# Kernel optimization log

Measured on AMD Instinct MI355X. Metric: run time of the kernel, lower is better.

Reference implementation:

```python
import jax, jax.numpy as jnp
import numpy as np

N, D, H = 4096, 1024, 16
HD = D // H  # 64
EPS = 1e-5


def setup_inputs() -> dict:
    key = jax.random.key(0)
    ks = jax.random.split(key, 12)
    lim = 1.0 / np.sqrt(D)
    def lin(kw, kb):
        W = jax.random.uniform(kw, (D, D), jnp.float32, -lim, lim)
        b = jax.random.uniform(kb, (D,), jnp.float32, -lim, lim)
        return W, b
    Wq, bq = lin(ks[0], ks[1])
    Wk, bk = lin(ks[2], ks[3])
    Wv, bv = lin(ks[4], ks[5])
    Wo, bo = lin(ks[6], ks[7])
    return {
        "query": jax.random.normal(ks[8], (N, D), jnp.float32),
        "key": jax.random.normal(ks[9], (N, D), jnp.float32),
        "value": jax.random.normal(ks[10], (N, D), jnp.float32),
        "Wq": Wq, "bq": bq, "Wk": Wk, "bk": bk,
        "Wv": Wv, "bv": bv, "Wo": Wo, "bo": bo,
        "q_norm_w": jnp.ones((HD,), jnp.float32),
        "k_norm_w": jnp.ones((HD,), jnp.float32),
    }


def _rmsnorm(x, w):
    # eqx.nn.RMSNorm: weight-only, eps=1e-5, over last dim
    inv = jax.lax.rsqrt(jnp.mean(x * x, axis=-1, keepdims=True) + EPS)
    return w * x * inv


def reference(query, key, value, Wq, bq, Wk, bk, Wv, bv, Wo, bo, q_norm_w, k_norm_w):
    n = query.shape[0]
    q = (query @ Wq.T + bq).reshape(n, H, HD)
    k = (key @ Wk.T + bk).reshape(n, H, HD)
    v = (value @ Wv.T + bv).reshape(n, H, HD)
    q = _rmsnorm(q, q_norm_w)
    k = _rmsnorm(k, k_norm_w)
    # scale=1.0: raw unscaled dot-product logits
    logits = jnp.einsum('qhd,khd->hqk', q, k)  # [H, N, N]
    probs = jax.nn.softmax(logits, axis=-1)
    attn = jnp.einsum('hqk,khd->qhd', probs, v).reshape(n, H * HD)
    return attn @ Wo.T + bo
```

## Files before the change

### kernel.cpp

```cpp
#include <hip/hip_runtime.h>
#include <stdint.h>
#include <stddef.h>

#define N_TOK 4096
#define DM    1024
#define NHEAD 16
#define HD    64

typedef __attribute__((ext_vector_type(8)))  short bf16x8;
typedef __attribute__((ext_vector_type(4)))  short bf16x4;
typedef __attribute__((ext_vector_type(4)))  float f32x4;
typedef __attribute__((ext_vector_type(16))) float f32x16;

static __device__ __forceinline__ float bf2f(short u) {
  union { unsigned int i; float f; } c;
  c.i = ((unsigned int)(unsigned short)u) << 16;
  return c.f;
}
static __device__ __forceinline__ unsigned short f2bf(float f) {
  union { float f; unsigned int i; } c; c.f = f;
  unsigned int x = c.i;
  return (unsigned short)((x + 0x7fffu + ((x >> 16) & 1u)) >> 16);
}
static __device__ __forceinline__ unsigned int cvtpk(float lo, float hi) {
  unsigned int d;
  asm("v_cvt_pk_bf16_f32 %0, %1, %2" : "=v"(d) : "v"(lo), "v"(hi));
  return d;
}
static __device__ __forceinline__ void plswap(unsigned int& a, unsigned int& b) {
  asm("v_permlane32_swap_b32 %0, %1" : "+v"(a), "+v"(b));
}
#if __has_builtin(__builtin_amdgcn_exp2f)
#define EXP2(x) __builtin_amdgcn_exp2f(x)
#else
#define EXP2(x) exp2f(x)
#endif
static __device__ __forceinline__ void gload16(const void* g, void* l) {
  __builtin_amdgcn_global_load_lds(
      (const __attribute__((address_space(1))) unsigned int*)g,
      (__attribute__((address_space(3))) unsigned int*)l, 16, 0, 0);
}

struct Cvt7 { const float* s[7]; unsigned short* d[7]; };
__global__ void cvt_all(Cvt7 a) {
  int u0 = blockIdx.x << 10;
  int seg, off;
  if (u0 < 1572864) { seg = u0 >> 19; off = u0 & 524287; }
  else { int j = u0 - 1572864; seg = 3 + (j >> 17); off = j & 131071; }
  const float* s = a.s[seg];
  unsigned short* dd = a.d[seg];
  int t = off + threadIdx.x;
#pragma unroll
  for (int j = 0; j < 4; ++j, t += 256) {
    const f32x4* sp = (const f32x4*)(s + (size_t)t * 8);
    f32x4 x = sp[0], y = sp[1];
    bf16x8 o;
    o[0] = (short)f2bf(x[0]); o[1] = (short)f2bf(x[1]);
    o[2] = (short)f2bf(x[2]); o[3] = (short)f2bf(x[3]);
    o[4] = (short)f2bf(y[0]); o[5] = (short)f2bf(y[1]);
    o[6] = (short)f2bf(y[2]); o[7] = (short)f2bf(y[3]);
    *(bf16x8*)(dd + (size_t)t * 8) = o;
  }
}

template <int MI>
static __device__ __forceinline__ void gemm_core(
    const unsigned short* __restrict__ A,
    const unsigned short* __restrict__ W,
    const float* __restrict__ bias,
    unsigned short* __restrict__ Cb,
    float* __restrict__ Cf,
    const float* __restrict__ nw,
    int Nn, int K, int mode, int m0, int n0)
{
  __shared__ __align__(16) unsigned short At[2][MI * 1024];
  __shared__ __align__(16) unsigned short Wt[2][128 * 32];
  const int tid  = threadIdx.x;
  const int wid  = tid >> 6, lane = tid & 63;
  const int lm   = lane & 15, lg = lane >> 4;
  const int wm   = (wid >> 1) * (MI * 16), wn = (wid & 1) * 64;
  const int CPW  = (MI * 2 + 8) / 4;

  f32x4 acc[MI][4];
#pragma unroll
  for (int i = 0; i < MI; ++i)
#pragma unroll
    for (int j = 0; j < 4; ++j) acc[i][j] = f32x4{0.f, 0.f, 0.f, 0.f};

  auto stage = [&](int b, int k0) {
#pragma unroll
    for (int i = 0; i < CPW; ++i) {
      int c = wid * CPW + i;
      if (c < MI * 2)
        gload16(A + (size_t)(m0 + c * 16 + (lane >> 2)) * K + k0 + (lane & 3) * 8,
                (char*)At + b * (MI * 2048) + c * 1024);
      else
        gload16(W + (size_t)(n0 + (c - MI * 2) * 16 + (lane >> 2)) * K + k0 + (lane & 3) * 8,
                (char*)Wt + b * 8192 + (c - MI * 2) * 1024);
    }
  };

  const int nk = K >> 5;
  stage(0, 0);
  __syncthreads();
  for (int kt = 0; kt < nk; ++kt) {
    const int cur = kt & 1;
    if (kt + 1 < nk) stage(cur ^ 1, (kt + 1) << 5);

    bf16x8 af[MI], bfr[4];
#pragma unroll
    for (int mi = 0; mi < MI; ++mi)
      af[mi] = *(const bf16x8*)&At[cur][(wm + mi * 16 + lm) * 32 + lg * 8];
#pragma unroll
    for (int ni = 0; ni < 4; ++ni)
      bfr[ni] = *(const bf16x8*)&Wt[cur][(wn + ni * 16 + lm) * 32 + lg * 8];
    __builtin_amdgcn_s_setprio(1);
#pragma unroll
    for (int mi = 0; mi < MI; ++mi)
#pragma unroll
      for (int ni = 0; ni < 4; ++ni)
        acc[mi][ni] = __builtin_amdgcn_mfma_f32_16x16x32_bf16(
            af[mi], bfr[ni], acc[mi][ni], 0, 0, 0);
    __builtin_amdgcn_s_setprio(0);
    __syncthreads();
  }

  float bv[4];
#pragma unroll
  for (int ni = 0; ni < 4; ++ni) bv[ni] = bias[n0 + wn + ni * 16 + lm];

  if (mode <= 1) {
#pragma unroll
    for (int mi = 0; mi < MI; ++mi)
#pragma unroll
      for (int ni = 0; ni < 4; ++ni) {
        int n = n0 + wn + ni * 16 + lm;
#pragma unroll
        for (int r = 0; r < 4; ++r) {
          int m = m0 + wm + mi * 16 + lg * 4 + r;
          float v = acc[mi][ni][r] + bv[ni];
          if (mode == 1) Cf[(size_t)m * Nn + n] = v;
          else           Cb[(size_t)m * Nn + n] = f2bf(v);
        }
      }
  } else if (mode == 2) {
    const int h = (n0 + wn) >> 6;
    float w_[4];
#pragma unroll
    for (int ni = 0; ni < 4; ++ni) w_[ni] = nw[ni * 16 + lm];
#pragma unroll
    for (int mi = 0; mi < MI; ++mi) {
      float t[4][4], ssq[4];
#pragma unroll
      for (int ni = 0; ni < 4; ++ni)
#pragma unroll
        for (int r = 0; r < 4; ++r) t[ni][r] = acc[mi][ni][r] + bv[ni];
#pragma unroll
      for (int r = 0; r < 4; ++r)
        ssq[r] = t[0][r]*t[0][r] + t[1][r]*t[1][r] + t[2][r]*t[2][r] + t[3][r]*t[3][r];
#pragma unroll
      for (int r = 0; r < 4; ++r) {
        ssq[r] += __shfl_xor(ssq[r], 1);
        ssq[r] += __shfl_xor(ssq[r], 2);
        ssq[r] += __shfl_xor(ssq[r], 4);
        ssq[r] += __shfl_xor(ssq[r], 8);
      }
#pragma unroll
      for (int r = 0; r < 4; ++r) {
        float iv = rsqrtf(ssq[r] * (1.f / 64.f) + 1e-5f);
        int n_ = m0 + wm + mi * 16 + lg * 4 + r;
#pragma unroll
        for (int ni = 0; ni < 4; ++ni) {
          int d = ni * 16 + lm;
          Cb[(size_t)h * (N_TOK * HD) + (size_t)n_ * HD + d] = f2bf(t[ni][r] * w_[ni] * iv);
        }
      }
    }
  } else {
    const int h = (n0 + wn) >> 6;
#pragma unroll
    for (int mi = 0; mi < MI; ++mi)
#pragma unroll
      for (int ni = 0; ni < 4; ++ni) {
        int d  = ni * 16 + lm;
        int nb = m0 + wm + mi * 16 + lg * 4;
        bf16x4 o;
#pragma unroll
        for (int r = 0; r < 4; ++r) o[r] = (short)f2bf(acc[mi][ni][r] + bv[ni]);
        *(bf16x4*)&Cb[(size_t)h * (HD * N_TOK) + (size_t)d * N_TOK + nb] = o;
      }
  }
}

__global__ __launch_bounds__(256, 3) void qkv_gemm(
    const unsigned short* __restrict__ a0, const unsigned short* __restrict__ a1,
    const unsigned short* __restrict__ a2,
    const unsigned short* __restrict__ w0, const unsigned short* __restrict__ w1,
    const unsigned short* __restrict__ w2,
    const float* __restrict__ b0, const float* __restrict__ b1,
    const float* __restrict__ b2,
    unsigned short* __restrict__ o0, unsigned short* __restrict__ o1,
    unsigned short* __restrict__ o2,
    const float* __restrict__ knw)
{
  const int z = blockIdx.z;
  const unsigned short* A = (z == 0) ? a0 : (z == 1) ? a1 : a2;
  const unsigned short* W = (z == 0) ? w0 : (z == 1) ? w1 : w2;
  const float* B          = (z == 0) ? b0 : (z == 1) ? b1 : b2;
  unsigned short* O       = (z == 0) ? o0 : (z == 1) ? o1 : o2;
  const int mode          = (z == 0) ? 0 : (z == 1) ? 2 : 3;
  gemm_core<4>(A, W, B, O, nullptr, knw, DM, DM, mode,
               blockIdx.y * 128, blockIdx.x * 128);
}

__global__ __launch_bounds__(256, 4) void out_gemm(
    const unsigned short* __restrict__ A, const unsigned short* __restrict__ W,
    const float* __restrict__ bias, float* __restrict__ Cf)
{
  gemm_core<2>(A, W, bias, nullptr, Cf, nullptr, DM, DM, 1,
               blockIdx.y * 64, blockIdx.x * 128);
}

__global__ __launch_bounds__(512, 4) void attn_kernel(
    const unsigned short* __restrict__ qb,
    const unsigned short* __restrict__ kn,
    const unsigned short* __restrict__ vt,
    const float* __restrict__ wq,
    unsigned short* __restrict__ ob)
{
  __shared__ __align__(16) unsigned short SM[2][2][2][4096];

  const int wg   = blockIdx.x;
  const int x_   = wg & 7, rest = wg >> 3;
  const int h    = x_ * 2 + (rest & 1);
  const int qt   = rest >> 1;
  const int tid  = threadIdx.x;
  const int wid  = tid >> 6, lane = tid & 63;
  const int g    = wid >> 2, wv = wid & 3;
  const int l31  = lane & 31, hi = lane >> 5;
  const int sl   = l31 & 7;
  const int qbase = qt * 128 + wv * 32;

  bf16x8 qf[4];
  {
    const unsigned short* qp = qb + (size_t)(qbase + l31) * DM + h * HD + hi * 8;
    float qv[32]; float ss = 0.f;
#pragma unroll
    for (int s = 0; s < 4; ++s) {
      bf16x8 raw = *(const bf16x8*)(qp + s * 16);
#pragma unroll
      for (int j = 0; j < 8; ++j) { float f = bf2f(raw[j]); qv[s*8+j] = f; ss += f*f; }
    }
    ss += __shfl_xor(ss, 32);
    float inv = rsqrtf(ss * (1.f / 64.f) + 1e-5f) * 1.44269504f;
#pragma unroll
    for (int s = 0; s < 4; ++s)
#pragma unroll
      for (int j = 0; j < 8; ++j)
        qf[s][j] = (short)f2bf(qv[s*8+j] * wq[s*16 + hi*8 + j] * inv);
  }

  int slot[4];
#pragma unroll
  for (int x = 0; x < 4; ++x) slot[x] = (((2*x + hi) ^ sl) << 4);
  const char* base = (const char*)SM + g * 32768 + l31 * 128;

  const char* gsrc[4];
  char*       ldst[4];
  long        gstep[4];
  {
    const char* knb = (const char*)kn + (size_t)h * (N_TOK * HD * 2);
    const char* vtb = (const char*)vt + (size_t)h * (HD * N_TOK * 2);
    char* smG = (char*)SM + g * 32768;
#pragma unroll
    for (int i = 0; i < 4; ++i) {
      int chunk = wv * 4 + i;
      int off   = (chunk & 7) * 1024 + lane * 16;
      int row   = off >> 7;
      int scol  = (off & 127) ^ ((row & 7) << 4);
      if (chunk < 8) {
        gsrc[i]  = knb + (size_t)(g * 2048 + row) * 128 + scol;
        gstep[i] = 64 * 128;
        ldst[i]  = smG + (chunk & 7) * 1024;
      } else {
        gsrc[i]  = vtb + (size_t)row * (N_TOK * 2) + g * 4096 + scol;
        gstep[i] = 64 * 2;
        ldst[i]  = smG + 8192 + (chunk & 7) * 1024;
      }
    }
  }

  f32x16 oacc[2], fz;
#pragma unroll
  for (int r = 0; r < 16; ++r) { oacc[0][r] = 0.f; oacc[1][r] = 0.f; fz[r] = 0.f; }
  float lsp[4] = {0.f, 0.f, 0.f, 0.f};

#pragma unroll
  for (int i = 0; i < 4; ++i) { gload16(gsrc[i], ldst[i]); gsrc[i] += gstep[i]; }
  __syncthreads();

  const int NT = 2048 / 64;
  for (int it = 0; it < NT; ++it) {
    const int cur = it & 1;
    if (it + 1 < NT) {
      const int nb = cur ^ 1;
#pragma unroll
      for (int i = 0; i < 4; ++i) {
        gload16(gsrc[i], ldst[i] + nb * 16384);
        gsrc[i] += gstep[i];
      }
    }
    const char* KB = base + cur * 16384;
    const char* VB = KB + 8192;

    f32x16 sc[2];
    __builtin_amdgcn_s_setprio(1);
#pragma unroll
    for (int kt = 0; kt < 2; ++kt) {
      bf16x8 kf0 = *(const bf16x8*)(KB + kt * 4096 + slot[0]);
      sc[kt] = __builtin_amdgcn_mfma_f32_32x32x16_bf16(kf0, qf[0], fz, 0, 0, 0);
#pragma unroll
      for (int s = 1; s < 4; ++s) {
        bf16x8 kf = *(const bf16x8*)(KB + kt * 4096 + slot[s]);
        sc[kt] = __builtin_amdgcn_mfma_f32_32x32x16_bf16(kf, qf[s], sc[kt], 0, 0, 0);
      }
    }
    __builtin_amdgcn_s_setprio(0);

#pragma unroll
    for (int kt = 0; kt < 2; ++kt) {
      float e[16];
#pragma unroll
      for (int r = 0; r < 16; ++r) { e[r] = EXP2(sc[kt][r]); lsp[r & 3] += e[r]; }
      unsigned int wpk[4][2];
#pragma unroll
      for (int b = 0; b < 4; ++b) {
        wpk[b][0] = cvtpk(e[4*b+0], e[4*b+1]);
        wpk[b][1] = cvtpk(e[4*b+2], e[4*b+3]);
      }
#pragma unroll
      for (int pr = 0; pr < 2; ++pr) {
        unsigned int x0 = wpk[2*pr][0], x1 = wpk[2*pr][1];
        unsigned int y0 = wpk[2*pr+1][0], y1 = wpk[2*pr+1][1];
        plswap(x0, y0);
        plswap(x1, y1);
        union { unsigned int u[4]; bf16x8 v; } pa;
        pa.u[0] = x0; pa.u[1] = x1; pa.u[2] = y0; pa.u[3] = y1;
        int ks = kt * 2 + pr;
        __builtin_amdgcn_s_setprio(1);
#pragma unroll
        for (int dt = 0; dt < 2; ++dt) {
          bf16x8 vf = *(const bf16x8*)(VB + dt * 4096 + slot[ks]);
          oacc[dt] = __builtin_amdgcn_mfma_f32_32x32x16_bf16(pa.v, vf, oacc[dt], 0, 0, 0);
        }
        __builtin_amdgcn_s_setprio(0);
      }
    }
    __syncthreads();
  }

  float ls = (lsp[0] + lsp[1]) + (lsp[2] + lsp[3]);
  ls += __shfl_xor(ls, 32);

  float* ex  = (float*)((char*)SM + 32768);
  float* lsx = (float*)SM;
  const int idx = wv * 64 + lane;
  if (g == 1) {
#pragma unroll
    for (int dt = 0; dt < 2; ++dt)
#pragma unroll
      for (int r = 0; r < 16; ++r)
        ex[(dt * 16 + r) * 256 + idx] = oacc[dt][r];
    lsx[idx] = ls;
  }
  __syncthreads();
  if (g == 0) {
#pragma unroll
    for (int dt = 0; dt < 2; ++dt)
#pragma unroll
      for (int r = 0; r < 16; ++r)
        oacc[dt][r] += ex[(dt * 16 + r) * 256 + idx];
    ls += lsx[idx];
    float il = 1.f / ls;
#pragma unroll
    for (int r = 0; r < 16; ++r) {
      int q = (r & 3) + 8 * (r >> 2) + 4 * hi;
      float ilr = __int_as_float(
          __builtin_amdgcn_ds_bpermute(q << 2, __float_as_int(il)));
      unsigned short* op = ob + (size_t)(qbase + q) * DM + h * HD + l31;
      op[0]  = f2bf(oacc[0][r] * ilr);
      op[32] = f2bf(oacc[1][r] * ilr);
    }
  }
}

extern "C" void kernel_launch(void* const* d_in, const int* in_sizes, int n_in,
                              void* d_out, int out_size, void* d_ws, size_t ws_size,
                              hipStream_t stream) {
  const float* query = (const float*)d_in[0];
  const float* key   = (const float*)d_in[1];
  const float* value = (const float*)d_in[2];
  const float* Wq    = (const float*)d_in[3];
  const float* bq    = (const float*)d_in[4];
  const float* Wk    = (const float*)d_in[5];
  const float* bk    = (const float*)d_in[6];
  const float* Wv    = (const float*)d_in[7];
  const float* bv    = (const float*)d_in[8];
  const float* Wo    = (const float*)d_in[9];
  const float* bo    = (const float*)d_in[10];
  const float* qnw   = (const float*)d_in[11];
  const float* knw   = (const float*)d_in[12];

  char* ws = (char*)d_ws;
  const size_t MB = 1024 * 1024;
  unsigned short* qpj = (unsigned short*)(ws + 0 * MB);
  unsigned short* Kn  = (unsigned short*)(ws + 8 * MB);
  unsigned short* Vt  = (unsigned short*)(ws + 16 * MB);
  unsigned short* wob = (unsigned short*)(ws + 24 * MB);
  unsigned short* wqb = (unsigned short*)(ws + 26 * MB);
  unsigned short* wkb = (unsigned short*)(ws + 28 * MB);
  unsigned short* wvb = (unsigned short*)(ws + 30 * MB);
  unsigned short* qbf = (unsigned short*)(ws + 32 * MB);
  unsigned short* kbf = (unsigned short*)(ws + 40 * MB);
  unsigned short* vbf = (unsigned short*)(ws + 48 * MB);
  unsigned short* apj = (unsigned short*)(ws + 56 * MB);

  Cvt7 ca;
  ca.s[0] = query; ca.d[0] = qbf;
  ca.s[1] = key;   ca.d[1] = kbf;
  ca.s[2] = value; ca.d[2] = vbf;
  ca.s[3] = Wq;    ca.d[3] = wqb;
  ca.s[4] = Wk;    ca.d[4] = wkb;
  ca.s[5] = Wv;    ca.d[5] = wvb;
  ca.s[6] = Wo;    ca.d[6] = wob;
  cvt_all<<<2048, 256, 0, stream>>>(ca);

  qkv_gemm<<<dim3(DM / 128, N_TOK / 128, 3), 256, 0, stream>>>(
      qbf, kbf, vbf, wqb, wkb, wvb, bq, bk, bv, qpj, Kn, Vt, knw);

  attn_kernel<<<512, 512, 0, stream>>>(qpj, Kn, Vt, qnw, apj);

  out_gemm<<<dim3(DM / 128, N_TOK / 64), 256, 0, stream>>>(apj, wob, bo, (float*)d_out);
}
```

Before: 154.7 us.

## Load V fragments directly from global and stage only K through LDS

V tiles are no longer staged through shared memory. Each lane now reads its V fragments straight from global memory into registers. Only K goes through LDS, using a 4-slot ring that is refilled two tiles at a time, so there is one barrier per two KV tiles instead of one per tile. The aim is to cut LDS traffic and barrier count. In exchange, the direct V loads are strided and uncoalesced and their latency is exposed inside compute, since they are issued at the start of each tile with no prefetch.

```diff
diff --git a/kernel.cpp b/kernel.cpp
--- a/kernel.cpp
+++ b/kernel.cpp
@@ -228,7 +228,7 @@
     const float* __restrict__ wq,
     unsigned short* __restrict__ ob)
 {
-  __shared__ __align__(16) unsigned short SM[2][2][2][4096];
+  __shared__ __align__(16) unsigned short Ksm[2][4][4096];
 
   const int wg   = blockIdx.x;
   const int x_   = wg & 7, rest = wg >> 3;
@@ -263,56 +263,45 @@
   int slot[4];
 #pragma unroll
   for (int x = 0; x < 4; ++x) slot[x] = (((2*x + hi) ^ sl) << 4);
-  const char* base = (const char*)SM + g * 32768 + l31 * 128;
-
-  const char* gsrc[4];
-  char*       ldst[4];
-  long        gstep[4];
+  const char* kbase = (const char*)Ksm + g * 32768 + l31 * 128;
+
+  const char* kgsrc[2];
+  char*       kldst[2];
   {
-    const char* knb = (const char*)kn + (size_t)h * (N_TOK * HD * 2);
-    const char* vtb = (const char*)vt + (size_t)h * (HD * N_TOK * 2);
-    char* smG = (char*)SM + g * 32768;
-#pragma unroll
-    for (int i = 0; i < 4; ++i) {
-      int chunk = wv * 4 + i;
-      int off   = (chunk & 7) * 1024 + lane * 16;
-      int row   = off >> 7;
-      int scol  = (off & 127) ^ ((row & 7) << 4);
-      if (chunk < 8) {
-        gsrc[i]  = knb + (size_t)(g * 2048 + row) * 128 + scol;
-        gstep[i] = 64 * 128;
-        ldst[i]  = smG + (chunk & 7) * 1024;
-      } else {
-        gsrc[i]  = vtb + (size_t)row * (N_TOK * 2) + g * 4096 + scol;
-        gstep[i] = 64 * 2;
-        ldst[i]  = smG + 8192 + (chunk & 7) * 1024;
-      }
-    }
-  }
+    const char* knb = (const char*)kn + (size_t)h * (N_TOK * HD * 2)
+                    + (size_t)g * 2048 * 128;
+#pragma unroll
+    for (int i = 0; i < 2; ++i) {
+      int c    = wv * 2 + i;
+      int off  = c * 1024 + lane * 16;
+      int row  = off >> 7;
+      int scol = (off & 127) ^ ((row & 7) << 4);
+      kgsrc[i] = knb + (size_t)row * 128 + scol;
+      kldst[i] = (char*)Ksm + g * 32768 + c * 1024;
+    }
+  }
+  const unsigned short* vb0 = vt + ((size_t)h * HD + l31) * N_TOK + g * 2048;
+  const unsigned short* vb1 = vb0 + (size_t)32 * N_TOK;
 
   f32x16 oacc[2], fz;
 #pragma unroll
   for (int r = 0; r < 16; ++r) { oacc[0][r] = 0.f; oacc[1][r] = 0.f; fz[r] = 0.f; }
   float lsp[4] = {0.f, 0.f, 0.f, 0.f};
 
-#pragma unroll
-  for (int i = 0; i < 4; ++i) { gload16(gsrc[i], ldst[i]); gsrc[i] += gstep[i]; }
-  __syncthreads();
-
-  const int NT = 2048 / 64;
-  for (int it = 0; it < NT; ++it) {
-    const int cur = it & 1;
-    if (it + 1 < NT) {
-      const int nb = cur ^ 1;
-#pragma unroll
-      for (int i = 0; i < 4; ++i) {
-        gload16(gsrc[i], ldst[i] + nb * 16384);
-        gsrc[i] += gstep[i];
-      }
-    }
-    const char* KB = base + cur * 16384;
-    const char* VB = KB + 8192;
-
+  auto stageK = [&](int t) {
+    gload16(kgsrc[0] + (size_t)t * 8192, kldst[0] + (t & 3) * 8192);
+    gload16(kgsrc[1] + (size_t)t * 8192, kldst[1] + (t & 3) * 8192);
+  };
+
+  auto compute = [&](int t) {
+    const char* KB  = kbase + (t & 3) * 8192;
+    const int   kvo = t * 64;
+    bf16x8 vr[2][4];
+#pragma unroll
+    for (int ks = 0; ks < 4; ++ks) {
+      vr[0][ks] = *(const bf16x8*)(vb0 + kvo + ks * 16 + hi * 8);
+      vr[1][ks] = *(const bf16x8*)(vb1 + kvo + ks * 16 + hi * 8);
+    }
     f32x16 sc[2];
     __builtin_amdgcn_s_setprio(1);
 #pragma unroll
@@ -326,7 +315,6 @@
       }
     }
     __builtin_amdgcn_s_setprio(0);
-
 #pragma unroll
     for (int kt = 0; kt < 2; ++kt) {
       float e[16];
@@ -346,24 +334,30 @@
         plswap(x1, y1);
         union { unsigned int u[4]; bf16x8 v; } pa;
         pa.u[0] = x0; pa.u[1] = x1; pa.u[2] = y0; pa.u[3] = y1;
-        int ks = kt * 2 + pr;
+        const int ks = kt * 2 + pr;
         __builtin_amdgcn_s_setprio(1);
-#pragma unroll
-        for (int dt = 0; dt < 2; ++dt) {
-          bf16x8 vf = *(const bf16x8*)(VB + dt * 4096 + slot[ks]);
-          oacc[dt] = __builtin_amdgcn_mfma_f32_32x32x16_bf16(pa.v, vf, oacc[dt], 0, 0, 0);
-        }
+        oacc[0] = __builtin_amdgcn_mfma_f32_32x32x16_bf16(pa.v, vr[0][ks], oacc[0], 0, 0, 0);
+        oacc[1] = __builtin_amdgcn_mfma_f32_32x32x16_bf16(pa.v, vr[1][ks], oacc[1], 0, 0, 0);
         __builtin_amdgcn_s_setprio(0);
       }
     }
+  };
+
+  stageK(0); stageK(1);
+  __syncthreads();
+
+  for (int p = 0; p < 16; ++p) {
+    if (p < 15) { stageK(2 * p + 2); stageK(2 * p + 3); }
+    compute(2 * p);
+    compute(2 * p + 1);
     __syncthreads();
   }
 
   float ls = (lsp[0] + lsp[1]) + (lsp[2] + lsp[3]);
   ls += __shfl_xor(ls, 32);
 
-  float* ex  = (float*)((char*)SM + 32768);
-  float* lsx = (float*)SM;
+  float* ex  = (float*)((char*)Ksm + 32768);
+  float* lsx = (float*)Ksm;
   const int idx = wv * 64 + lane;
   if (g == 1) {
 #pragma unroll
```

New measurement: 264.0 us. 1.71x slower.
